# Kernel tuning notes

Hardware: AMD Instinct MI355X
Metric: run time of the kernel (lower is better)

The kernel has to match this reference:

```python
import jax, jax.numpy as jnp
import numpy as np

EPS_BN = 1e-5
EPS_COS = 1e-8
N, E, D = 50000, 1600000, 128
HGC, LG, NUM_CLASSES, EIN, PAE_H = 64, 4, 2, 12, 128


def setup_inputs() -> dict:
    key = jax.random.key(0)
    ks = jax.random.split(key, 16)
    kaiming = lambda k, fi, fo: jax.random.normal(k, (fi, fo), jnp.float32) * (2.0 / fi) ** 0.5
    glorot = lambda k, shape: jax.random.normal(k, shape, jnp.float32) * (2.0 / (shape[-2] + shape[-1])) ** 0.5
    inp = {}
    inp["features"] = jax.random.normal(ks[0], (N, D), jnp.float32)
    inp["edge_index"] = jax.random.randint(ks[1], (2, E), 0, N, jnp.int32)
    inp["edgenet_input"] = jax.random.normal(ks[2], (E, EIN), jnp.float32)
    # PAE parser: Linear(6,128) -> ReLU -> BN(128) -> Dropout -> Linear(128,128)
    inp["pae_w1"] = kaiming(ks[3], EIN // 2, PAE_H)
    inp["pae_b1"] = jnp.zeros((PAE_H,), jnp.float32)
    inp["pae_bn_g"] = jnp.ones((PAE_H,), jnp.float32)
    inp["pae_bn_b"] = jnp.zeros((PAE_H,), jnp.float32)
    inp["pae_bn_rm"] = jnp.zeros((PAE_H,), jnp.float32)
    inp["pae_bn_rv"] = jnp.ones((PAE_H,), jnp.float32)
    inp["pae_w2"] = kaiming(ks[4], PAE_H, PAE_H)
    inp["pae_b2"] = jnp.zeros((PAE_H,), jnp.float32)
    # ChebConv weights, K=3, bias=False: [K, in, out]
    inp["cheb_w0"] = glorot(ks[5], (3, D, HGC))
    inp["cheb_w1"] = glorot(ks[6], (3, HGC, HGC))
    inp["cheb_w2"] = glorot(ks[7], (3, HGC, HGC))
    inp["cheb_w3"] = glorot(ks[8], (3, HGC, HGC))
    # classifier: Linear(lg*hgc=256, 256) -> ReLU -> BN(256) -> Linear(256, num_classes)
    CLS_IN = LG * HGC
    inp["cls_w1"] = kaiming(ks[9], CLS_IN, 256)
    inp["cls_b1"] = jnp.zeros((256,), jnp.float32)
    inp["cls_bn_g"] = jnp.ones((256,), jnp.float32)
    inp["cls_bn_b"] = jnp.zeros((256,), jnp.float32)
    inp["cls_bn_rm"] = jnp.zeros((256,), jnp.float32)
    inp["cls_bn_rv"] = jnp.ones((256,), jnp.float32)
    inp["cls_w2"] = kaiming(ks[10], 256, NUM_CLASSES)
    inp["cls_b2"] = jnp.zeros((NUM_CLASSES,), jnp.float32)
    return inp


def _bn_eval(h, g, b, rm, rv):
    return (h - rm) * jax.lax.rsqrt(rv + EPS_BN) * g + b


def _pae(x, w1, b1, g, b, rm, rv, w2, b2):
    half = w1.shape[0]
    def enc(z):
        h = jax.nn.relu(z @ w1 + b1)
        h = _bn_eval(h, g, b, rm, rv)
        return h @ w2 + b2                      # [E, PAE_H]
    h1, h2 = enc(x[:, :half]), enc(x[:, half:])
    num = jnp.sum(h1 * h2, axis=1)
    den = jnp.maximum(jnp.linalg.norm(h1, axis=1) * jnp.linalg.norm(h2, axis=1), EPS_COS)
    return (num / den + 1.0) * 0.5              # cosine sim mapped to [0, 1]


def _cheb_conv(x, W, row, col, norm, n_nodes):
    # (the +I from L and the -I self-loops with fill=-1 cancel in the propagation)
    def lhat(z):
        return jax.ops.segment_sum(norm[:, None] * z[col], row, num_segments=n_nodes)
    Tx0 = x
    Tx1 = lhat(Tx0)
    Tx2 = 2.0 * lhat(Tx1) - Tx0
    return Tx0 @ W[0] + Tx1 @ W[1] + Tx2 @ W[2]


def reference(features, edge_index, edgenet_input,
              pae_w1, pae_b1, pae_bn_g, pae_bn_b, pae_bn_rm, pae_bn_rv, pae_w2, pae_b2,
              cheb_w0, cheb_w1, cheb_w2, cheb_w3,
              cls_w1, cls_b1, cls_bn_g, cls_bn_b, cls_bn_rm, cls_bn_rv, cls_w2, cls_b2):
    n_nodes = features.shape[0]
    row, col = edge_index[0], edge_index[1]
    # learned edge weights
    edge_weight = _pae(edgenet_input, pae_w1, pae_b1, pae_bn_g, pae_bn_b,
                       pae_bn_rm, pae_bn_rv, pae_w2, pae_b2)
    # sym-normalized (negative) adjacency weights of the scaled Laplacian
    deg = jax.ops.segment_sum(edge_weight, row, num_segments=n_nodes)
    dis = jnp.where(deg > 0, jax.lax.rsqrt(jnp.where(deg > 0, deg, 1.0)), 0.0)
    norm = -dis[row] * edge_weight * dis[col]
    # GCN stack with jumping-knowledge concat (eval mode: dropout is identity)
    h = jax.nn.relu(_cheb_conv(features, cheb_w0, row, col, norm, n_nodes))
    jk = h
    for W in (cheb_w1, cheb_w2, cheb_w3):
        h = jax.nn.relu(_cheb_conv(h, W, row, col, norm, n_nodes))
        jk = jnp.concatenate((jk, h), axis=1)
    # classifier head
    z = jax.nn.relu(jk @ cls_w1 + cls_b1)
    z = _bn_eval(z, cls_bn_g, cls_bn_b, cls_bn_rm, cls_bn_rv)
    logit = z @ cls_w2 + cls_b2
    return (jk, logit, edge_weight)
```

## Files before the change

### kernel.cpp

```cpp
#include <hip/hip_runtime.h>

#define NN 50000
#define EE 1600000

using u16 = unsigned short;
using u32 = unsigned int;
using u64 = unsigned long long;

typedef float f32x4 __attribute__((ext_vector_type(4)));
typedef __bf16 bf16x8 __attribute__((ext_vector_type(8)));
typedef unsigned short u16x8 __attribute__((ext_vector_type(8)));

struct alignas(8) U16x4 { u16 a, b, c, d; };
struct PtrTab { const void* p[20]; };

#define OW1 0
#define OB1 768
#define OG 896
#define OBB 1024
#define ORM 1152
#define ORV 1280
#define OW2 1408
#define OB2 17792
#define OCH0 17920
#define OCH1 42496
#define OCH2 54784
#define OCH3 67072
#define OCW1 79360
#define OCB1 144896
#define OCG 145152
#define OCBB 145408
#define OCRM 145664
#define OCRV 145920
#define OCW2 146176
#define OCB2 146688
#define OTOT 146690

#define LG_OFF ((size_t)NN * 256)
#define EW_OFF ((size_t)NN * 256 + (size_t)NN * 2)

__device__ __forceinline__ float bf2f(u16 u) { return __builtin_bit_cast(float, (u32)u << 16); }
__device__ __forceinline__ float bfl(u32 u) { return __builtin_bit_cast(float, u << 16); }
__device__ __forceinline__ float bfh(u32 u) { return __builtin_bit_cast(float, u & 0xffff0000u); }
__device__ __forceinline__ u16 f2bf(float f) {
    u32 u = __builtin_bit_cast(u32, f);
    return (u16)((u + 0x7fffu + ((u >> 16) & 1u)) >> 16);
}

__global__ __launch_bounds__(256) void k_detect(const u16* __restrict__ f, int* __restrict__ flag) {
    __shared__ int bad;
    if (threadIdx.x == 0) bad = 0;
    __syncthreads();
    u16 u = f[threadIdx.x];
    int e = (u >> 7) & 0xFF;
    if (e >= 0x90) atomicAdd(&bad, 1);
    __syncthreads();
    if (threadIdx.x == 0) flag[0] = (bad < 16) ? 1 : 0;
}

__global__ __launch_bounds__(256) void k_wconv(PtrTab tab, const int* __restrict__ flag,
                                               float* __restrict__ wpad) {
    const int SZ[20] = {768, 128, 128, 128, 128, 128, 16384, 128, 24576, 12288, 12288, 12288,
                        65536, 256, 256, 256, 256, 256, 512, 2};
    const int OF[20] = {OW1, OB1, OG, OBB, ORM, ORV, OW2, OB2, OCH0, OCH1, OCH2, OCH3,
                        OCW1, OCB1, OCG, OCBB, OCRM, OCRV, OCW2, OCB2};
    int a = blockIdx.x;
    int n = SZ[a];
    float* dst = wpad + OF[a];
    if (flag[0] != 0) {
        const u16* s = (const u16*)tab.p[a];
        for (int i = threadIdx.x; i < n; i += 256) dst[i] = bf2f(s[i]);
    } else {
        const float* s = (const float*)tab.p[a];
        for (int i = threadIdx.x; i < n; i += 256) dst[i] = s[i];
    }
}

__global__ __launch_bounds__(128) void k_fold(const float* __restrict__ wpad,
                                              u16* __restrict__ W2s, float* __restrict__ b2p) {
    const float* g = wpad + OG;
    const float* b = wpad + OBB;
    const float* rm = wpad + ORM;
    const float* rv = wpad + ORV;
    const float* w2 = wpad + OW2;
    const float* b2 = wpad + OB2;
    int blk = blockIdx.x, tid = threadIdx.x;
    if (blk < 32) {
        int kc = blk >> 3, jt = blk & 7;
        int lane = tid & 63, jh = tid >> 6;
        for (int jj = 0; jj < 4; jj++) {
            int j = jh * 4 + jj;
            int k = kc * 32 + (lane >> 4) * 8 + j;
            int jcol = jt * 16 + (lane & 15);
            float s = g[k] * rsqrtf(rv[k] + 1e-5f);
            W2s[((kc * 8 + jt) * 64 + lane) * 8 + j] = f2bf(s * w2[k * 128 + jcol]);
        }
    } else {
        if (tid < 128) {
            int j = tid;
            float acc = b2[j];
            for (int k = 0; k < 128; k++) {
                float s = g[k] * rsqrtf(rv[k] + 1e-5f);
                float t = b[k] - rm[k] * s;
                acc += t * w2[k * 128 + j];
            }
            b2p[j] = acc;
        }
    }
}

__global__ __launch_bounds__(256) void k_foldc(const float* __restrict__ wpad,
                                               u16* __restrict__ W1c, float* __restrict__ w2p,
                                               float* __restrict__ b2p2) {
    int tid = threadIdx.x;
    if (blockIdx.x < 64) {
        const float* w1 = wpad + OCW1;
        int base = blockIdx.x * 1024 + tid * 4;
#pragma unroll
        for (int u = 0; u < 4; u++) {
            int gi = base + u;
            int j = gi & 7;
            int lane = (gi >> 3) & 63;
            int ct = (gi >> 9) & 15;
            int kc2 = (gi >> 13) & 1;
            int l = gi >> 14;
            int k = l * 64 + kc2 * 32 + ((lane >> 4) & 3) * 8 + j;
            int col = ct * 16 + (lane & 15);
            W1c[gi] = f2bf(w1[k * 256 + col]);
        }
    } else {
        __shared__ float red[8];
        int j = tid;
        float s = wpad[OCG + j] * rsqrtf(wpad[OCRV + j] + 1e-5f);
        float t = wpad[OCBB + j] - wpad[OCRM + j] * s;
        float w0 = wpad[OCW2 + j * 2], w1v = wpad[OCW2 + j * 2 + 1];
        w2p[j * 2] = s * w0;
        w2p[j * 2 + 1] = s * w1v;
        float c0 = t * w0, c1 = t * w1v;
#pragma unroll
        for (int off = 1; off < 64; off <<= 1) {
            c0 += __shfl_xor(c0, off);
            c1 += __shfl_xor(c1, off);
        }
        int wv = tid >> 6, lane = tid & 63;
        if (lane == 0) { red[wv * 2] = c0; red[wv * 2 + 1] = c1; }
        __syncthreads();
        if (tid == 0) b2p2[0] = wpad[OCB2] + red[0] + red[2] + red[4] + red[6];
        if (tid == 1) b2p2[1] = wpad[OCB2 + 1] + red[1] + red[3] + red[5] + red[7];
    }
}

__global__ __launch_bounds__(256) void k_foldw(const float* __restrict__ wpad,
                                               u16* __restrict__ Wf0, u16* __restrict__ Wf1,
                                               u16* __restrict__ Wf2, u16* __restrict__ Wf3) {
    int b = blockIdx.x, tid = threadIdx.x;
    const float* src;
    u16* dst;
    int nkt;
    if (b < 24)      { src = wpad + OCH0; dst = Wf0; nkt = 12; }
    else if (b < 36) { src = wpad + OCH1; dst = Wf1; b -= 24; nkt = 6; }
    else if (b < 48) { src = wpad + OCH2; dst = Wf2; b -= 36; nkt = 6; }
    else             { src = wpad + OCH3; dst = Wf3; b -= 48; nkt = 6; }
    int base = b * 1024 + tid * 4;
#pragma unroll
    for (int u = 0; u < 4; u++) {
        int gi = base + u;
        int jj = gi & 7;
        int lane = (gi >> 3) & 63;
        int ct = (gi >> 9) & 3;
        int kt = gi >> 11;
        if (kt < nkt) {
            int k = kt * 32 + ((lane >> 4) & 3) * 8 + jj;
            int col = ct * 16 + (lane & 15);
            dst[gi] = f2bf(src[k * 64 + col]);
        }
    }
}

__global__ __launch_bounds__(256) void k_x0(const void* __restrict__ feat, const int* __restrict__ flag,
                                            u16* __restrict__ X0) {
    int i = blockIdx.x * 256 + threadIdx.x;
    if (flag[0] != 0) {
        ((uint4*)X0)[i] = ((const uint4*)feat)[i];
    } else {
        const float4* f = (const float4*)feat;
        float4 a = f[2 * i], b = f[2 * i + 1];
        u16x8 o;
        o[0] = f2bf(a.x); o[1] = f2bf(a.y); o[2] = f2bf(a.z); o[3] = f2bf(a.w);
        o[4] = f2bf(b.x); o[5] = f2bf(b.y); o[6] = f2bf(b.z); o[7] = f2bf(b.w);
        ((uint4*)X0)[i] = __builtin_bit_cast(uint4, o);
    }
}

__global__ __launch_bounds__(256, 3) void k_pae(const void* __restrict__ zin, const float* __restrict__ wpad,
                                                const u16* __restrict__ W2sg, const float* __restrict__ b2p,
                                                const int* __restrict__ ei, const int* __restrict__ flag,
                                                float* __restrict__ ewf, void* __restrict__ dout,
                                                u64* __restrict__ dc) {
    __shared__ __align__(16) u16 sW2[16384];
    __shared__ __align__(16) float sW1k[1024];
    __shared__ float sB2[128];
    int tid = threadIdx.x;
    for (int i = tid; i < 8192; i += 256) ((u32*)sW2)[i] = ((const u32*)W2sg)[i];
    for (int i = tid; i < 1024; i += 256) {
        int k = i >> 3, m = i & 7;
        float v = 0.f;
        if (m < 6) v = wpad[OW1 + m * 128 + k];
        else if (m == 6) v = wpad[OB1 + k];
        int sw = ((k >> 3) & 3) << 4;
        *(float*)((char*)sW1k + ((k * 32 + m * 4) ^ sw)) = v;
    }
    if (tid < 128) sB2[tid] = b2p[tid];
    __syncthreads();

    bool isbf = flag[0] != 0;
    int wv = __builtin_amdgcn_readfirstlane(tid >> 6);
    int lane = tid & 63;
    int quad = lane >> 4, lrow = lane & 15, jc = lane & 15;
    int sq = quad << 4;
    int gw = blockIdx.x * 4 + wv;
    const int ngroups = EE / 16;
    const int gstep = gridDim.x * 4;

    uint2 pb0, pb1, pb2;
    float4 pf0, pf1, pf2;
    if (gw < ngroups) {
        if (isbf) {
            const uint2* zp = (const uint2*)((const u16*)zin + (size_t)(gw * 16 + lrow) * 12);
            pb0 = zp[0]; pb1 = zp[1]; pb2 = zp[2];
        } else {
            const float4* zp = (const float4*)((const float*)zin + (size_t)(gw * 16 + lrow) * 12);
            pf0 = zp[0]; pf1 = zp[1]; pf2 = zp[2];
        }
    }

#pragma unroll 1
    for (int gidx = gw; gidx < ngroups; gidx += gstep) {
        int e0 = gidx * 16;
        float z1[6], z2[6];
        if (isbf) {
            z1[0] = bfl(pb0.x); z1[1] = bfh(pb0.x); z1[2] = bfl(pb0.y); z1[3] = bfh(pb0.y);
            z1[4] = bfl(pb1.x); z1[5] = bfh(pb1.x);
            z2[0] = bfl(pb1.y); z2[1] = bfh(pb1.y); z2[2] = bfl(pb2.x); z2[3] = bfh(pb2.x);
            z2[4] = bfl(pb2.y); z2[5] = bfh(pb2.y);
        } else {
            z1[0] = pf0.x; z1[1] = pf0.y; z1[2] = pf0.z; z1[3] = pf0.w; z1[4] = pf1.x; z1[5] = pf1.y;
            z2[0] = pf1.z; z2[1] = pf1.w; z2[2] = pf2.x; z2[3] = pf2.y; z2[4] = pf2.z; z2[5] = pf2.w;
        }
        int gn = gidx + gstep;
        if (gn < ngroups) {
            if (isbf) {
                const uint2* zp = (const uint2*)((const u16*)zin + (size_t)(gn * 16 + lrow) * 12);
                pb0 = zp[0]; pb1 = zp[1]; pb2 = zp[2];
            } else {
                const float4* zp = (const float4*)((const float*)zin + (size_t)(gn * 16 + lrow) * 12);
                pf0 = zp[0]; pf1 = zp[1]; pf2 = zp[2];
            }
        }
        int rows[4];
        if (jc == 0) {
#pragma unroll
            for (int r = 0; r < 4; r++) rows[r] = ei[e0 + quad * 4 + r];
        }

        bf16x8 a1f[4], a2f[4];
#pragma unroll
        for (int kc = 0; kc < 4; kc++) {
            int kbase = kc * 32 + quad * 8;
            u32 r1[4], r2[4];
#pragma unroll
            for (int jh = 0; jh < 4; jh++) {
                int k = kbase + 2 * jh;
                const char* bp = (const char*)sW1k;
                float4 wa = *(const float4*)(bp + ((k * 32) ^ sq));
                float4 wb = *(const float4*)(bp + ((k * 32 + 16) ^ sq));
                float4 wc = *(const float4*)(bp + (((k + 1) * 32) ^ sq));
                float4 wd = *(const float4*)(bp + (((k + 1) * 32 + 16) ^ sq));
                float sA1 = wb.z, sA2 = wb.z, sB1 = wd.z, sB2v = wd.z;
                sA1 = fmaf(z1[0], wa.x, sA1); sA2 = fmaf(z2[0], wa.x, sA2);
                sA1 = fmaf(z1[1], wa.y, sA1); sA2 = fmaf(z2[1], wa.y, sA2);
                sA1 = fmaf(z1[2], wa.z, sA1); sA2 = fmaf(z2[2], wa.z, sA2);
                sA1 = fmaf(z1[3], wa.w, sA1); sA2 = fmaf(z2[3], wa.w, sA2);
                sA1 = fmaf(z1[4], wb.x, sA1); sA2 = fmaf(z2[4], wb.x, sA2);
                sA1 = fmaf(z1[5], wb.y, sA1); sA2 = fmaf(z2[5], wb.y, sA2);
                sB1 = fmaf(z1[0], wc.x, sB1); sB2v = fmaf(z2[0], wc.x, sB2v);
                sB1 = fmaf(z1[1], wc.y, sB1); sB2v = fmaf(z2[1], wc.y, sB2v);
                sB1 = fmaf(z1[2], wc.z, sB1); sB2v = fmaf(z2[2], wc.z, sB2v);
                sB1 = fmaf(z1[3], wc.w, sB1); sB2v = fmaf(z2[3], wc.w, sB2v);
                sB1 = fmaf(z1[4], wd.x, sB1); sB2v = fmaf(z2[4], wd.x, sB2v);
                sB1 = fmaf(z1[5], wd.y, sB1); sB2v = fmaf(z2[5], wd.y, sB2v);
                sA1 = fmaxf(sA1, 0.f); sA2 = fmaxf(sA2, 0.f);
                sB1 = fmaxf(sB1, 0.f); sB2v = fmaxf(sB2v, 0.f);
                u32 o1, o2;
                asm("v_cvt_pk_bf16_f32 %0, %1, %2" : "=v"(o1) : "v"(sA1), "v"(sB1));
                asm("v_cvt_pk_bf16_f32 %0, %1, %2" : "=v"(o2) : "v"(sA2), "v"(sB2v));
                r1[jh] = o1; r2[jh] = o2;
            }
            uint4 u1v = {r1[0], r1[1], r1[2], r1[3]};
            uint4 u2v = {r2[0], r2[1], r2[2], r2[3]};
            a1f[kc] = __builtin_bit_cast(bf16x8, u1v);
            a2f[kc] = __builtin_bit_cast(bf16x8, u2v);
        }

        float num[4] = {0, 0, 0, 0}, q1[4] = {0, 0, 0, 0}, q2[4] = {0, 0, 0, 0};
#pragma unroll 1
        for (int jt = 0; jt < 8; jt++) {
            f32x4 acc1 = {0.f, 0.f, 0.f, 0.f}, acc2 = {0.f, 0.f, 0.f, 0.f};
#pragma unroll
            for (int kc = 0; kc < 4; kc++) {
                bf16x8 bb = *reinterpret_cast<const bf16x8*>(&sW2[((kc * 8 + jt) * 64 + lane) * 8]);
                acc1 = __builtin_amdgcn_mfma_f32_16x16x32_bf16(a1f[kc], bb, acc1, 0, 0, 0);
                acc2 = __builtin_amdgcn_mfma_f32_16x16x32_bf16(a2f[kc], bb, acc2, 0, 0, 0);
            }
            float bbias = sB2[jt * 16 + jc];
#pragma unroll
            for (int r = 0; r < 4; r++) {
                float h1 = acc1[r] + bbias;
                float h2 = acc2[r] + bbias;
                num[r] = fmaf(h1, h2, num[r]);
                q1[r] = fmaf(h1, h1, q1[r]);
                q2[r] = fmaf(h2, h2, q2[r]);
            }
        }
#pragma unroll
        for (int off = 1; off < 16; off <<= 1) {
#pragma unroll
            for (int r = 0; r < 4; r++) {
                num[r] += __shfl_xor(num[r], off);
                q1[r] += __shfl_xor(q1[r], off);
                q2[r] += __shfl_xor(q2[r], off);
            }
        }
        if (jc == 0) {
#pragma unroll
            for (int r = 0; r < 4; r++) {
                int e = e0 + quad * 4 + r;
                float den = fmaxf(sqrtf(q1[r]) * sqrtf(q2[r]), 1e-8f);
                float wgt = (num[r] / den + 1.f) * 0.5f;
                if (!(wgt == wgt)) wgt = 0.5f;
                ewf[e] = wgt;
                if (isbf) ((u16*)dout)[EW_OFF + e] = f2bf(wgt);
                else ((float*)dout)[EW_OFF + e] = wgt;
                u32 fx = (u32)(wgt * 8388608.f + 0.5f);
                atomicAdd(dc + rows[r], (((u64)1) << 32) | (u64)fx);
            }
        }
    }
}

__global__ __launch_bounds__(1024) void k_scan(const u64* __restrict__ dc,
                                               int* __restrict__ offs, float* __restrict__ dis) {
    __shared__ int wsum[16];
    __shared__ int carry;
    int tid = threadIdx.x;
    int wv = tid >> 6, lane = tid & 63;
    if (tid == 0) carry = 0;
    __syncthreads();
    for (int c = 0; c < 49; c++) {
        int i = c * 1024 + tid;
        u64 v64 = (i < NN) ? dc[i] : 0ull;
        int v = (int)(v64 >> 32);
        if (i < NN) {
            float d = (float)(u32)v64 * (1.f / 8388608.f);
            dis[i] = d > 0.f ? rsqrtf(d) : 0.f;
        }
        int x = v;
#pragma unroll
        for (int off = 1; off < 64; off <<= 1) {
            int t = __shfl_up(x, off);
            if (lane >= off) x += t;
        }
        if (lane == 63) wsum[wv] = x;
        __syncthreads();
        if (tid < 16) {
            int s = wsum[tid];
#pragma unroll
            for (int off = 1; off < 16; off <<= 1) {
                int t = __shfl_up(s, off, 16);
                if (tid >= off) s += t;
            }
            wsum[tid] = s;
        }
        __syncthreads();
        int base = carry + (wv > 0 ? wsum[wv - 1] : 0);
        if (i < NN) offs[i] = base + x - v;
        __syncthreads();
        if (tid == 0) carry += wsum[15];
        __syncthreads();
    }
    if (tid == 0) offs[NN] = carry;
}

__global__ __launch_bounds__(256) void k_csr(const int* __restrict__ ei, const float* __restrict__ ewf,
                                             const float* __restrict__ dis, const int* __restrict__ offs,
                                             int* __restrict__ cursor, uint2* __restrict__ csr_meta) {
    int e = blockIdx.x * 256 + threadIdx.x;
    int r = ei[e], c = ei[EE + e];
    float wgt = ewf[e];
    int pos = offs[r] + atomicAdd(cursor + r, 1);
    float nrm = -dis[r] * wgt * dis[c];
    csr_meta[pos] = make_uint2((u32)c, __builtin_bit_cast(u32, nrm));
}

template <int F>
__global__ __launch_bounds__(256) void k_prop(const u16* __restrict__ src, const uint2* __restrict__ csr_meta,
                                              const int* __restrict__ offs,
                                              u16* __restrict__ out, const u16* __restrict__ base,
                                              float alpha, float beta) {
    int lane = threadIdx.x & 63;
    int wv = threadIdx.x >> 6;
    int node = blockIdx.x * 4 + wv;
    int s = offs[node], e = offs[node + 1];

    if (F == 128) {
        int sub = lane >> 4;
        int fl = lane & 15;
        const uint4* sv = (const uint4*)src;
        float a[8] = {0, 0, 0, 0, 0, 0, 0, 0};
        int p = s;
        if (p + 7 < e) {
            uint2 m0 = csr_meta[p + sub];
            uint2 m1 = csr_meta[p + 4 + sub];
            while (true) {
                uint4 v0 = sv[(size_t)m0.x * 16 + fl];
                uint4 v1 = sv[(size_t)m1.x * 16 + fl];
                float w0 = __builtin_bit_cast(float, m0.y);
                float w1 = __builtin_bit_cast(float, m1.y);
                p += 8;
                bool more = (p + 7 < e);
                if (more) {
                    m0 = csr_meta[p + sub];
                    m1 = csr_meta[p + 4 + sub];
                }
                a[0] = fmaf(w0, bfl(v0.x), a[0]); a[1] = fmaf(w0, bfh(v0.x), a[1]);
                a[2] = fmaf(w0, bfl(v0.y), a[2]); a[3] = fmaf(w0, bfh(v0.y), a[3]);
                a[4] = fmaf(w0, bfl(v0.z), a[4]); a[5] = fmaf(w0, bfh(v0.z), a[5]);
                a[6] = fmaf(w0, bfl(v0.w), a[6]); a[7] = fmaf(w0, bfh(v0.w), a[7]);
                a[0] = fmaf(w1, bfl(v1.x), a[0]); a[1] = fmaf(w1, bfh(v1.x), a[1]);
                a[2] = fmaf(w1, bfl(v1.y), a[2]); a[3] = fmaf(w1, bfh(v1.y), a[3]);
                a[4] = fmaf(w1, bfl(v1.z), a[4]); a[5] = fmaf(w1, bfh(v1.z), a[5]);
                a[6] = fmaf(w1, bfl(v1.w), a[6]); a[7] = fmaf(w1, bfh(v1.w), a[7]);
                if (!more) break;
            }
        }
        if (p + 3 < e) {
            uint2 m0 = csr_meta[p + sub];
            uint4 v0 = sv[(size_t)m0.x * 16 + fl];
            float w0 = __builtin_bit_cast(float, m0.y);
            a[0] = fmaf(w0, bfl(v0.x), a[0]); a[1] = fmaf(w0, bfh(v0.x), a[1]);
            a[2] = fmaf(w0, bfl(v0.y), a[2]); a[3] = fmaf(w0, bfh(v0.y), a[3]);
            a[4] = fmaf(w0, bfl(v0.z), a[4]); a[5] = fmaf(w0, bfh(v0.z), a[5]);
            a[6] = fmaf(w0, bfl(v0.w), a[6]); a[7] = fmaf(w0, bfh(v0.w), a[7]);
            p += 4;
        }
#pragma unroll
        for (int i = 0; i < 8; i++) {
            a[i] += __shfl_xor(a[i], 16);
            a[i] += __shfl_xor(a[i], 32);
        }
        if (sub == 0) {
            for (; p < e; p++) {
                uint2 m0 = csr_meta[p];
                uint4 v = sv[(size_t)m0.x * 16 + fl];
                float w = __builtin_bit_cast(float, m0.y);
                a[0] = fmaf(w, bfl(v.x), a[0]); a[1] = fmaf(w, bfh(v.x), a[1]);
                a[2] = fmaf(w, bfl(v.y), a[2]); a[3] = fmaf(w, bfh(v.y), a[3]);
                a[4] = fmaf(w, bfl(v.z), a[4]); a[5] = fmaf(w, bfh(v.z), a[5]);
                a[6] = fmaf(w, bfl(v.w), a[6]); a[7] = fmaf(w, bfh(v.w), a[7]);
            }
            float o[8];
#pragma unroll
            for (int i = 0; i < 8; i++) o[i] = alpha * a[i];
            if (beta != 0.f) {
                uint4 bv = ((const uint4*)base)[(size_t)node * 16 + fl];
                o[0] = fmaf(beta, bfl(bv.x), o[0]); o[1] = fmaf(beta, bfh(bv.x), o[1]);
                o[2] = fmaf(beta, bfl(bv.y), o[2]); o[3] = fmaf(beta, bfh(bv.y), o[3]);
                o[4] = fmaf(beta, bfl(bv.z), o[4]); o[5] = fmaf(beta, bfh(bv.z), o[5]);
                o[6] = fmaf(beta, bfl(bv.w), o[6]); o[7] = fmaf(beta, bfh(bv.w), o[7]);
            }
            uint4 ov;
            ov.x = (u32)f2bf(o[0]) | ((u32)f2bf(o[1]) << 16);
            ov.y = (u32)f2bf(o[2]) | ((u32)f2bf(o[3]) << 16);
            ov.z = (u32)f2bf(o[4]) | ((u32)f2bf(o[5]) << 16);
            ov.w = (u32)f2bf(o[6]) | ((u32)f2bf(o[7]) << 16);
            ((uint4*)out)[(size_t)node * 16 + fl] = ov;
        }
    } else {
        int sub = lane >> 3;
        int fl = lane & 7;
        const uint4* sv = (const uint4*)src;
        float a[8] = {0, 0, 0, 0, 0, 0, 0, 0};
        int p = s;
        if (p + 15 < e) {
            uint2 m0 = csr_meta[p + sub];
            uint2 m1 = csr_meta[p + 8 + sub];
            while (true) {
                uint4 v0 = sv[(size_t)m0.x * 8 + fl];
                uint4 v1 = sv[(size_t)m1.x * 8 + fl];
                float w0 = __builtin_bit_cast(float, m0.y);
                float w1 = __builtin_bit_cast(float, m1.y);
                p += 16;
                bool more = (p + 15 < e);
                if (more) {
                    m0 = csr_meta[p + sub];
                    m1 = csr_meta[p + 8 + sub];
                }
                a[0] = fmaf(w0, bfl(v0.x), a[0]); a[1] = fmaf(w0, bfh(v0.x), a[1]);
                a[2] = fmaf(w0, bfl(v0.y), a[2]); a[3] = fmaf(w0, bfh(v0.y), a[3]);
                a[4] = fmaf(w0, bfl(v0.z), a[4]); a[5] = fmaf(w0, bfh(v0.z), a[5]);
                a[6] = fmaf(w0, bfl(v0.w), a[6]); a[7] = fmaf(w0, bfh(v0.w), a[7]);
                a[0] = fmaf(w1, bfl(v1.x), a[0]); a[1] = fmaf(w1, bfh(v1.x), a[1]);
                a[2] = fmaf(w1, bfl(v1.y), a[2]); a[3] = fmaf(w1, bfh(v1.y), a[3]);
                a[4] = fmaf(w1, bfl(v1.z), a[4]); a[5] = fmaf(w1, bfh(v1.z), a[5]);
                a[6] = fmaf(w1, bfl(v1.w), a[6]); a[7] = fmaf(w1, bfh(v1.w), a[7]);
                if (!more) break;
            }
        }
        if (p + 7 < e) {
            uint2 m0 = csr_meta[p + sub];
            uint4 v0 = sv[(size_t)m0.x * 8 + fl];
            float w0 = __builtin_bit_cast(float, m0.y);
            a[0] = fmaf(w0, bfl(v0.x), a[0]); a[1] = fmaf(w0, bfh(v0.x), a[1]);
            a[2] = fmaf(w0, bfl(v0.y), a[2]); a[3] = fmaf(w0, bfh(v0.y), a[3]);
            a[4] = fmaf(w0, bfl(v0.z), a[4]); a[5] = fmaf(w0, bfh(v0.z), a[5]);
            a[6] = fmaf(w0, bfl(v0.w), a[6]); a[7] = fmaf(w0, bfh(v0.w), a[7]);
            p += 8;
        }
#pragma unroll
        for (int i = 0; i < 8; i++) {
            a[i] += __shfl_xor(a[i], 8);
            a[i] += __shfl_xor(a[i], 16);
            a[i] += __shfl_xor(a[i], 32);
        }
        if (sub == 0) {
            for (; p < e; p++) {
                uint2 m0 = csr_meta[p];
                uint4 v = sv[(size_t)m0.x * 8 + fl];
                float w = __builtin_bit_cast(float, m0.y);
                a[0] = fmaf(w, bfl(v.x), a[0]); a[1] = fmaf(w, bfh(v.x), a[1]);
                a[2] = fmaf(w, bfl(v.y), a[2]); a[3] = fmaf(w, bfh(v.y), a[3]);
                a[4] = fmaf(w, bfl(v.z), a[4]); a[5] = fmaf(w, bfh(v.z), a[5]);
                a[6] = fmaf(w, bfl(v.w), a[6]); a[7] = fmaf(w, bfh(v.w), a[7]);
            }
            float o[8];
#pragma unroll
            for (int i = 0; i < 8; i++) o[i] = alpha * a[i];
            if (beta != 0.f) {
                uint4 bv = ((const uint4*)base)[(size_t)node * 8 + fl];
                o[0] = fmaf(beta, bfl(bv.x), o[0]); o[1] = fmaf(beta, bfh(bv.x), o[1]);
                o[2] = fmaf(beta, bfl(bv.y), o[2]); o[3] = fmaf(beta, bfh(bv.y), o[3]);
                o[4] = fmaf(beta, bfl(bv.z), o[4]); o[5] = fmaf(beta, bfh(bv.z), o[5]);
                o[6] = fmaf(beta, bfl(bv.w), o[6]); o[7] = fmaf(beta, bfh(bv.w), o[7]);
            }
            uint4 ov;
            ov.x = (u32)f2bf(o[0]) | ((u32)f2bf(o[1]) << 16);
            ov.y = (u32)f2bf(o[2]) | ((u32)f2bf(o[3]) << 16);
            ov.z = (u32)f2bf(o[4]) | ((u32)f2bf(o[5]) << 16);
            ov.w = (u32)f2bf(o[6]) | ((u32)f2bf(o[7]) << 16);
            ((uint4*)out)[(size_t)node * 8 + fl] = ov;
        }
    }
}

template <int F>
__global__ __launch_bounds__(256) void k_gemm(const u16* __restrict__ X0, const u16* __restrict__ X1,
                                              const u16* __restrict__ X2, const u16* __restrict__ Wf,
                                              u16* __restrict__ Hout, void* __restrict__ jk, int jkoff,
                                              const int* __restrict__ flag) {
    constexpr int KT = (3 * F) / 32;
    __shared__ __align__(16) u16 sB[KT * 4 * 64 * 8];
    int tid = threadIdx.x;
    for (int i = tid; i < KT * 4 * 64 * 4; i += 256) ((u32*)sB)[i] = ((const u32*)Wf)[i];
    __syncthreads();

    bool isbf = flag[0] != 0;
    int wv = __builtin_amdgcn_readfirstlane(tid >> 6);
    int lane = tid & 63;
    int quad = lane >> 4, jc = lane & 15;
    int pair = wv >> 1;
    int half = wv & 1;
    int nb = blockIdx.x * 32 + pair * 16;
    int row = nb + jc;
    if (row > NN - 1) row = NN - 1;

    uint4 av[KT];
#pragma unroll
    for (int kt = 0; kt < KT; kt++) {
        int kg = kt * 32 + quad * 8;
        const u16* Xp;
        int kk;
        if (kg < F) { Xp = X0; kk = kg; }
        else if (kg < 2 * F) { Xp = X1; kk = kg - F; }
        else { Xp = X2; kk = kg - 2 * F; }
        av[kt] = *(const uint4*)(Xp + (size_t)row * F + kk);
    }

    f32x4 acc0 = {0.f, 0.f, 0.f, 0.f}, acc1 = {0.f, 0.f, 0.f, 0.f};
#pragma unroll
    for (int kt = 0; kt < KT; kt++) {
        bf16x8 af = __builtin_bit_cast(bf16x8, av[kt]);
        bf16x8 b0 = *reinterpret_cast<const bf16x8*>(&sB[((kt * 4 + half * 2 + 0) * 64 + lane) * 8]);
        bf16x8 b1 = *reinterpret_cast<const bf16x8*>(&sB[((kt * 4 + half * 2 + 1) * 64 + lane) * 8]);
        acc0 = __builtin_amdgcn_mfma_f32_16x16x32_bf16(af, b0, acc0, 0, 0, 0);
        acc1 = __builtin_amdgcn_mfma_f32_16x16x32_bf16(af, b1, acc1, 0, 0, 0);
    }

#pragma unroll
    for (int ct = 0; ct < 2; ct++) {
        f32x4 a = ct ? acc1 : acc0;
        int j = (half * 2 + ct) * 16 + jc;
#pragma unroll
        for (int r = 0; r < 4; r++) {
            int n = nb + quad * 4 + r;
            if (n < NN) {
                float v = fmaxf(a[r], 0.f);
                Hout[(size_t)n * 64 + j] = f2bf(v);
                if (isbf) ((u16*)jk)[(size_t)n * 256 + jkoff + j] = f2bf(v);
                else ((float*)jk)[(size_t)n * 256 + jkoff + j] = v;
            }
        }
    }
}

__global__ __launch_bounds__(256) void k_cls(const u16* __restrict__ h0, const u16* __restrict__ h1,
                                             const u16* __restrict__ h2, const u16* __restrict__ h3,
                                             const u16* __restrict__ W1c, const float* __restrict__ wpad,
                                             const float* __restrict__ w2p, const float* __restrict__ b2p2,
                                             const int* __restrict__ flag, void* __restrict__ dout) {
    __shared__ __align__(16) u16 sB[16384];
    __shared__ float sb1[256];
    __shared__ float sw2[512];
    __shared__ float sb2[2];
    __shared__ float part[4][16][2];
    int tid = threadIdx.x;
    if (tid < 256) sb1[tid] = wpad[OCB1 + tid];
    for (int i = tid; i < 512; i += 256) sw2[i] = w2p[i];
    if (tid < 2) sb2[tid] = b2p2[tid];

    int wv = __builtin_amdgcn_readfirstlane(tid >> 6);
    int lane = tid & 63;
    int quad = lane >> 4, jc = lane & 15;
    int pair = wv >> 1;
    int half = wv & 1;
    int nb = blockIdx.x * 32 + pair * 16;

    f32x4 acc[8] = {{0.f, 0.f, 0.f, 0.f}, {0.f, 0.f, 0.f, 0.f}, {0.f, 0.f, 0.f, 0.f}, {0.f, 0.f, 0.f, 0.f},
                    {0.f, 0.f, 0.f, 0.f}, {0.f, 0.f, 0.f, 0.f}, {0.f, 0.f, 0.f, 0.f}, {0.f, 0.f, 0.f, 0.f}};
    const u16* hs[4] = {h0, h1, h2, h3};

    int row = nb + jc;
    if (row > NN - 1) row = NN - 1;

#pragma unroll 1
    for (int l = 0; l < 4; l++) {
        __syncthreads();
        const u32* src = (const u32*)W1c + l * 8192;
        for (int i = tid; i < 8192; i += 256) ((u32*)sB)[i] = src[i];
        __syncthreads();
        const uint4* rp = (const uint4*)(hs[l] + (size_t)row * 64);
        uint4 a0u = rp[quad], a1u = rp[4 + quad];
        bf16x8 af0 = __builtin_bit_cast(bf16x8, a0u);
        bf16x8 af1 = __builtin_bit_cast(bf16x8, a1u);
#pragma unroll
        for (int jt = 0; jt < 8; jt++) {
            int ct = half * 8 + jt;
            bf16x8 b0 = *reinterpret_cast<const bf16x8*>(&sB[((0 * 16 + ct) * 64 + lane) * 8]);
            bf16x8 b1f = *reinterpret_cast<const bf16x8*>(&sB[((1 * 16 + ct) * 64 + lane) * 8]);
            acc[jt] = __builtin_amdgcn_mfma_f32_16x16x32_bf16(af0, b0, acc[jt], 0, 0, 0);
            acc[jt] = __builtin_amdgcn_mfma_f32_16x16x32_bf16(af1, b1f, acc[jt], 0, 0, 0);
        }
    }

    float p0[4] = {0, 0, 0, 0}, p1[4] = {0, 0, 0, 0};
#pragma unroll
    for (int jt = 0; jt < 8; jt++) {
        int j = (half * 8 + jt) * 16 + jc;
        float b1v = sb1[j], wa = sw2[2 * j], wb = sw2[2 * j + 1];
#pragma unroll
        for (int r = 0; r < 4; r++) {
            float h = fmaxf(acc[jt][r] + b1v, 0.f);
            p0[r] = fmaf(h, wa, p0[r]);
            p1[r] = fmaf(h, wb, p1[r]);
        }
    }
#pragma unroll
    for (int off = 1; off < 16; off <<= 1) {
#pragma unroll
        for (int r = 0; r < 4; r++) {
            p0[r] += __shfl_xor(p0[r], off);
            p1[r] += __shfl_xor(p1[r], off);
        }
    }
    if (jc == 0) {
#pragma unroll
        for (int r = 0; r < 4; r++) {
            part[wv][quad * 4 + r][0] = p0[r];
            part[wv][quad * 4 + r][1] = p1[r];
        }
    }
    __syncthreads();
    if (tid < 32) {
        int rl = tid & 15, p = tid >> 4;
        int n = blockIdx.x * 32 + tid;
        if (n < NN) {
            float l0 = part[2 * p][rl][0] + part[2 * p + 1][rl][0] + sb2[0];
            float l1 = part[2 * p][rl][1] + part[2 * p + 1][rl][1] + sb2[1];
            if (flag[0] != 0) {
                u32 pack = (u32)f2bf(l0) | ((u32)f2bf(l1) << 16);
                *(u32*)((u16*)dout + LG_OFF + (size_t)n * 2) = pack;
            } else {
                float2 o = {l0, l1};
                *(float2*)((float*)dout + LG_OFF + (size_t)n * 2) = o;
            }
        }
    }
}

extern "C" void kernel_launch(void* const* d_in, const int* in_sizes, int n_in,
                              void* d_out, int out_size, void* d_ws, size_t ws_size,
                              hipStream_t stream) {
    const void* features = d_in[0];
    const int* ei = (const int*)d_in[1];
    const void* zin = d_in[2];

    char* w = (char*)d_ws;
    auto alloc = [&](size_t bytes) -> void* {
        void* p = (void*)w;
        w += (bytes + 255) & ~(size_t)255;
        return p;
    };
    u16* X0 = (u16*)alloc((size_t)NN * 128 * 2);
    u16* Tx1 = (u16*)alloc((size_t)NN * 128 * 2);
    u16* Tx2 = (u16*)alloc((size_t)NN * 128 * 2);
    u16* h0 = (u16*)alloc((size_t)NN * 64 * 2);
    u16* h1 = (u16*)alloc((size_t)NN * 64 * 2);
    u16* h2 = (u16*)alloc((size_t)NN * 64 * 2);
    u16* h3 = (u16*)alloc((size_t)NN * 64 * 2);
    float* ewf = (float*)alloc((size_t)EE * 4);
    uint2* csr_meta = (uint2*)alloc((size_t)EE * 8);
    u64* dc = (u64*)alloc((size_t)NN * 8);
    int* cursor = (int*)alloc((size_t)NN * 4);
    float* dis = (float*)alloc((size_t)NN * 4);
    int* offs = (int*)alloc((size_t)(NN + 1) * 4);
    u16* W2s = (u16*)alloc((size_t)16384 * 2);
    float* b2p = (float*)alloc((size_t)128 * 4);
    u16* W1c = (u16*)alloc((size_t)65536 * 2);
    float* w2p = (float*)alloc((size_t)512 * 4);
    float* b2p2 = (float*)alloc((size_t)2 * 4);
    u16* Wf0 = (u16*)alloc((size_t)24576 * 2);
    u16* Wf1 = (u16*)alloc((size_t)12288 * 2);
    u16* Wf2 = (u16*)alloc((size_t)12288 * 2);
    u16* Wf3 = (u16*)alloc((size_t)12288 * 2);
    float* wpad = (float*)alloc((size_t)OTOT * 4);
    int* flag = (int*)alloc(256);

    hipMemsetAsync(dc, 0, (size_t)((char*)dis - (char*)dc), stream);

    PtrTab tab;
    for (int i = 0; i < 20; i++) tab.p[i] = d_in[3 + i];

    k_detect<<<1, 256, 0, stream>>>((const u16*)features, flag);
    k_wconv<<<20, 256, 0, stream>>>(tab, flag, wpad);
    k_fold<<<33, 128, 0, stream>>>(wpad, W2s, b2p);
    k_foldc<<<65, 256, 0, stream>>>(wpad, W1c, w2p, b2p2);
    k_foldw<<<60, 256, 0, stream>>>(wpad, Wf0, Wf1, Wf2, Wf3);
    k_x0<<<3125, 256, 0, stream>>>(features, flag, X0);
    k_pae<<<768, 256, 0, stream>>>(zin, wpad, W2s, b2p, ei, flag, ewf, d_out, dc);
    k_scan<<<1, 1024, 0, stream>>>(dc, offs, dis);
    k_csr<<<EE / 256, 256, 0, stream>>>(ei, ewf, dis, offs, cursor, csr_meta);

    k_prop<128><<<12500, 256, 0, stream>>>(X0, csr_meta, offs, Tx1, nullptr, 1.f, 0.f);
    k_prop<128><<<12500, 256, 0, stream>>>(Tx1, csr_meta, offs, Tx2, X0, 2.f, -1.f);
    k_gemm<128><<<1563, 256, 0, stream>>>(X0, Tx1, Tx2, Wf0, h0, d_out, 0, flag);
    k_prop<64><<<12500, 256, 0, stream>>>(h0, csr_meta, offs, Tx1, nullptr, 1.f, 0.f);
    k_prop<64><<<12500, 256, 0, stream>>>(Tx1, csr_meta, offs, Tx2, h0, 2.f, -1.f);
    k_gemm<64><<<1563, 256, 0, stream>>>(h0, Tx1, Tx2, Wf1, h1, d_out, 64, flag);
    k_prop<64><<<12500, 256, 0, stream>>>(h1, csr_meta, offs, Tx1, nullptr, 1.f, 0.f);
    k_prop<64><<<12500, 256, 0, stream>>>(Tx1, csr_meta, offs, Tx2, h1, 2.f, -1.f);
    k_gemm<64><<<1563, 256, 0, stream>>>(h1, Tx1, Tx2, Wf2, h2, d_out, 128, flag);
    k_prop<64><<<12500, 256, 0, stream>>>(h2, csr_meta, offs, Tx1, nullptr, 1.f, 0.f);
    k_prop<64><<<12500, 256, 0, stream>>>(Tx1, csr_meta, offs, Tx2, h2, 2.f, -1.f);
    k_gemm<64><<<1563, 256, 0, stream>>>(h2, Tx1, Tx2, Wf3, h3, d_out, 192, flag);

    k_cls<<<1563, 256, 0, stream>>>(h0, h1, h2, h3, W1c, wpad, w2p, b2p2, flag, d_out);
    (void)in_sizes; (void)n_in; (void)out_size; (void)ws_size;
}
```

Baseline: 1.011 ms.

## Compute PAE first layer with MFMA instead of scalar FMAs from LDS

Moves the PAE first linear layer (6->128 with bias and ReLU) from per-lane scalar FMAs that read swizzled weights from shared memory onto bf16 MFMA instructions. W1 is held in registers with the K dimension zero-padded and the bias is folded into the accumulator. The fold kernel reorders the W2 k-index so that the MFMA output layout feeds straight into the second-layer A fragments. This cuts VALU and LDS work per edge group but rounds the inputs and W1 to bf16, costs more registers (8 uint4 plus 8 f32x4 held in the loop), and wastes most of each MFMA's K dimension on padding.

```diff
diff --git a/kernel.cpp b/kernel.cpp
--- a/kernel.cpp
+++ b/kernel.cpp
@@ -88,9 +88,10 @@
     if (blk < 32) {
         int kc = blk >> 3, jt = blk & 7;
         int lane = tid & 63, jh = tid >> 6;
+        int q = lane >> 4;
         for (int jj = 0; jj < 4; jj++) {
             int j = jh * 4 + jj;
-            int k = kc * 32 + (lane >> 4) * 8 + j;
+            int k = kc * 32 + ((j < 4) ? (q * 4 + j) : (16 + q * 4 + (j - 4)));
             int jcol = jt * 16 + (lane & 15);
             float s = g[k] * rsqrtf(rv[k] + 1e-5f);
             W2s[((kc * 8 + jt) * 64 + lane) * 8 + j] = f2bf(s * w2[k * 128 + jcol]);
@@ -198,18 +199,9 @@
                                                 float* __restrict__ ewf, void* __restrict__ dout,
                                                 u64* __restrict__ dc) {
     __shared__ __align__(16) u16 sW2[16384];
-    __shared__ __align__(16) float sW1k[1024];
     __shared__ float sB2[128];
     int tid = threadIdx.x;
     for (int i = tid; i < 8192; i += 256) ((u32*)sW2)[i] = ((const u32*)W2sg)[i];
-    for (int i = tid; i < 1024; i += 256) {
-        int k = i >> 3, m = i & 7;
-        float v = 0.f;
-        if (m < 6) v = wpad[OW1 + m * 128 + k];
-        else if (m == 6) v = wpad[OB1 + k];
-        int sw = ((k >> 3) & 3) << 4;
-        *(float*)((char*)sW1k + ((k * 32 + m * 4) ^ sw)) = v;
-    }
     if (tid < 128) sB2[tid] = b2p[tid];
     __syncthreads();
 
@@ -217,7 +209,24 @@
     int wv = __builtin_amdgcn_readfirstlane(tid >> 6);
     int lane = tid & 63;
     int quad = lane >> 4, lrow = lane & 15, jc = lane & 15;
-    int sq = quad << 4;
+    u32 qm = (quad == 0) ? 0xffffffffu : 0u;
+
+    uint4 w1f[8];
+    f32x4 cb[8];
+#pragma unroll
+    for (int kt = 0; kt < 8; kt++) {
+        u32 a = 0, b = 0, c = 0;
+        if (quad == 0) {
+            int col = kt * 16 + lrow;
+            a = (u32)f2bf(wpad[OW1 + 0 * 128 + col]) | ((u32)f2bf(wpad[OW1 + 1 * 128 + col]) << 16);
+            b = (u32)f2bf(wpad[OW1 + 2 * 128 + col]) | ((u32)f2bf(wpad[OW1 + 3 * 128 + col]) << 16);
+            c = (u32)f2bf(wpad[OW1 + 4 * 128 + col]) | ((u32)f2bf(wpad[OW1 + 5 * 128 + col]) << 16);
+        }
+        w1f[kt] = (uint4){a, b, c, 0u};
+#pragma unroll
+        for (int r = 0; r < 4; r++) cb[kt][r] = wpad[OB1 + kt * 16 + quad * 4 + r];
+    }
+
     int gw = blockIdx.x * 4 + wv;
     const int ngroups = EE / 16;
     const int gstep = gridDim.x * 4;
@@ -263,43 +272,60 @@
             for (int r = 0; r < 4; r++) rows[r] = ei[e0 + quad * 4 + r];
         }
 
+        u32 za0, za1, za2, zb0, zb1, zb2;
+        asm("v_cvt_pk_bf16_f32 %0, %1, %2" : "=v"(za0) : "v"(z1[0]), "v"(z1[1]));
+        asm("v_cvt_pk_bf16_f32 %0, %1, %2" : "=v"(za1) : "v"(z1[2]), "v"(z1[3]));
+        asm("v_cvt_pk_bf16_f32 %0, %1, %2" : "=v"(za2) : "v"(z1[4]), "v"(z1[5]));
+        asm("v_cvt_pk_bf16_f32 %0, %1, %2" : "=v"(zb0) : "v"(z2[0]), "v"(z2[1]));
+        asm("v_cvt_pk_bf16_f32 %0, %1, %2" : "=v"(zb1) : "v"(z2[2]), "v"(z2[3]));
+        asm("v_cvt_pk_bf16_f32 %0, %1, %2" : "=v"(zb2) : "v"(z2[4]), "v"(z2[5]));
+        uint4 zu1 = {za0 & qm, za1 & qm, za2 & qm, 0u};
+        uint4 zu2 = {zb0 & qm, zb1 & qm, zb2 & qm, 0u};
+        bf16x8 zf1 = __builtin_bit_cast(bf16x8, zu1);
+        bf16x8 zf2 = __builtin_bit_cast(bf16x8, zu2);
+
         bf16x8 a1f[4], a2f[4];
-#pragma unroll
-        for (int kc = 0; kc < 4; kc++) {
-            int kbase = kc * 32 + quad * 8;
-            u32 r1[4], r2[4];
-#pragma unroll
-            for (int jh = 0; jh < 4; jh++) {
-                int k = kbase + 2 * jh;
-                const char* bp = (const char*)sW1k;
-                float4 wa = *(const float4*)(bp + ((k * 32) ^ sq));
-                float4 wb = *(const float4*)(bp + ((k * 32 + 16) ^ sq));
-                float4 wc = *(const float4*)(bp + (((k + 1) * 32) ^ sq));
-                float4 wd = *(const float4*)(bp + (((k + 1) * 32 + 16) ^ sq));
-                float sA1 = wb.z, sA2 = wb.z, sB1 = wd.z, sB2v = wd.z;
-                sA1 = fmaf(z1[0], wa.x, sA1); sA2 = fmaf(z2[0], wa.x, sA2);
-                sA1 = fmaf(z1[1], wa.y, sA1); sA2 = fmaf(z2[1], wa.y, sA2);
-                sA1 = fmaf(z1[2], wa.z, sA1); sA2 = fmaf(z2[2], wa.z, sA2);
-                sA1 = fmaf(z1[3], wa.w, sA1); sA2 = fmaf(z2[3], wa.w, sA2);
-                sA1 = fmaf(z1[4], wb.x, sA1); sA2 = fmaf(z2[4], wb.x, sA2);
-                sA1 = fmaf(z1[5], wb.y, sA1); sA2 = fmaf(z2[5], wb.y, sA2);
-                sB1 = fmaf(z1[0], wc.x, sB1); sB2v = fmaf(z2[0], wc.x, sB2v);
-                sB1 = fmaf(z1[1], wc.y, sB1); sB2v = fmaf(z2[1], wc.y, sB2v);
-                sB1 = fmaf(z1[2], wc.z, sB1); sB2v = fmaf(z2[2], wc.z, sB2v);
-                sB1 = fmaf(z1[3], wc.w, sB1); sB2v = fmaf(z2[3], wc.w, sB2v);
-                sB1 = fmaf(z1[4], wd.x, sB1); sB2v = fmaf(z2[4], wd.x, sB2v);
-                sB1 = fmaf(z1[5], wd.y, sB1); sB2v = fmaf(z2[5], wd.y, sB2v);
-                sA1 = fmaxf(sA1, 0.f); sA2 = fmaxf(sA2, 0.f);
-                sB1 = fmaxf(sB1, 0.f); sB2v = fmaxf(sB2v, 0.f);
-                u32 o1, o2;
-                asm("v_cvt_pk_bf16_f32 %0, %1, %2" : "=v"(o1) : "v"(sA1), "v"(sB1));
-                asm("v_cvt_pk_bf16_f32 %0, %1, %2" : "=v"(o2) : "v"(sA2), "v"(sB2v));
-                r1[jh] = o1; r2[jh] = o2;
-            }
-            uint4 u1v = {r1[0], r1[1], r1[2], r1[3]};
-            uint4 u2v = {r2[0], r2[1], r2[2], r2[3]};
-            a1f[kc] = __builtin_bit_cast(bf16x8, u1v);
-            a2f[kc] = __builtin_bit_cast(bf16x8, u2v);
+        {
+            f32x4 c1[8];
+#pragma unroll
+            for (int kt = 0; kt < 8; kt++)
+                c1[kt] = __builtin_amdgcn_mfma_f32_16x16x32_bf16(
+                    __builtin_bit_cast(bf16x8, w1f[kt]), zf1, cb[kt], 0, 0, 0);
+#pragma unroll
+            for (int kc = 0; kc < 4; kc++) {
+                float h0 = fmaxf(c1[2 * kc][0], 0.f), h1 = fmaxf(c1[2 * kc][1], 0.f);
+                float h2 = fmaxf(c1[2 * kc][2], 0.f), h3 = fmaxf(c1[2 * kc][3], 0.f);
+                float h4 = fmaxf(c1[2 * kc + 1][0], 0.f), h5 = fmaxf(c1[2 * kc + 1][1], 0.f);
+                float h6 = fmaxf(c1[2 * kc + 1][2], 0.f), h7 = fmaxf(c1[2 * kc + 1][3], 0.f);
+                u32 p0, p1, p2, p3;
+                asm("v_cvt_pk_bf16_f32 %0, %1, %2" : "=v"(p0) : "v"(h0), "v"(h1));
+                asm("v_cvt_pk_bf16_f32 %0, %1, %2" : "=v"(p1) : "v"(h2), "v"(h3));
+                asm("v_cvt_pk_bf16_f32 %0, %1, %2" : "=v"(p2) : "v"(h4), "v"(h5));
+                asm("v_cvt_pk_bf16_f32 %0, %1, %2" : "=v"(p3) : "v"(h6), "v"(h7));
+                uint4 au = {p0, p1, p2, p3};
+                a1f[kc] = __builtin_bit_cast(bf16x8, au);
+            }
+        }
+        {
+            f32x4 c2[8];
+#pragma unroll
+            for (int kt = 0; kt < 8; kt++)
+                c2[kt] = __builtin_amdgcn_mfma_f32_16x16x32_bf16(
+                    __builtin_bit_cast(bf16x8, w1f[kt]), zf2, cb[kt], 0, 0, 0);
+#pragma unroll
+            for (int kc = 0; kc < 4; kc++) {
+                float h0 = fmaxf(c2[2 * kc][0], 0.f), h1 = fmaxf(c2[2 * kc][1], 0.f);
+                float h2 = fmaxf(c2[2 * kc][2], 0.f), h3 = fmaxf(c2[2 * kc][3], 0.f);
+                float h4 = fmaxf(c2[2 * kc + 1][0], 0.f), h5 = fmaxf(c2[2 * kc + 1][1], 0.f);
+                float h6 = fmaxf(c2[2 * kc + 1][2], 0.f), h7 = fmaxf(c2[2 * kc + 1][3], 0.f);
+                u32 p0, p1, p2, p3;
+                asm("v_cvt_pk_bf16_f32 %0, %1, %2" : "=v"(p0) : "v"(h0), "v"(h1));
+                asm("v_cvt_pk_bf16_f32 %0, %1, %2" : "=v"(p1) : "v"(h2), "v"(h3));
+                asm("v_cvt_pk_bf16_f32 %0, %1, %2" : "=v"(p2) : "v"(h4), "v"(h5));
+                asm("v_cvt_pk_bf16_f32 %0, %1, %2" : "=v"(p3) : "v"(h6), "v"(h7));
+                uint4 au = {p0, p1, p2, p3};
+                a2f[kc] = __builtin_bit_cast(bf16x8, au);
+            }
         }
 
         float num[4] = {0, 0, 0, 0}, q1[4] = {0, 0, 0, 0}, q2[4] = {0, 0, 0, 0};
```

Result: faster. 978.5 us (-3.2%).
